# Optimization experiments

Measured on AMD Instinct MI355X. Metric: run time of the kernel, lower is better.

## Reference

```python
import jax, jax.numpy as jnp
import numpy as np
import math

B, S, D, H, COND = 4, 2048, 768, 12, 128
DH = D // H
MLP = 4 * D
EPS = 1e-5


def setup_inputs() -> dict:
    key = jax.random.key(0)
    ks = jax.random.split(key, 10)
    s = 0.02  # init scale for weights
    x = jax.random.normal(ks[0], (B, S, D), jnp.float32)
    c = jax.random.normal(ks[1], (B, COND), jnp.float32)
    # rotary tables, layout (1, S, 3, 1, DH) per module docstring
    pos = jnp.arange(S, dtype=jnp.float32)
    inv_freq = 1.0 / (10000.0 ** (jnp.arange(0, DH, 2, dtype=jnp.float32) / DH))
    ang = pos[:, None] * inv_freq[None, :]            # (S, DH/2)
    cos = jnp.concatenate([jnp.cos(ang), jnp.cos(ang)], -1)  # (S, DH)
    sin = jnp.concatenate([jnp.sin(ang), jnp.sin(ang)], -1)
    cos = jnp.broadcast_to(cos[None, :, None, None, :], (1, S, 3, 1, DH))
    sin = jnp.broadcast_to(sin[None, :, None, None, :], (1, S, 3, 1, DH))
    return {
        "x": x,
        "cos": cos,
        "sin": sin,
        "c": c,
        "ln1_w": jnp.ones((D,), jnp.float32),
        "W_qkv": s * jax.random.normal(ks[2], (3 * D, D), jnp.float32),
        "W_out": s * jax.random.normal(ks[3], (D, D), jnp.float32),
        "W_mlp1": s * jax.random.normal(ks[4], (MLP, D), jnp.float32),
        "b_mlp1": jnp.zeros((MLP,), jnp.float32),
        "W_mlp2": s * jax.random.normal(ks[5], (D, MLP), jnp.float32),
        "b_mlp2": jnp.zeros((D,), jnp.float32),
        "ln2_w": jnp.ones((D,), jnp.float32),
        "W_ada": s * jax.random.normal(ks[6], (6 * D, COND), jnp.float32),
        "b_ada": jnp.zeros((6 * D,), jnp.float32),
    }


def _ln(x, w):
    # LayerNorm with weight only (no bias), computed in fp32 like the original
    xf = x.astype(jnp.float32)
    mu = xf.mean(-1, keepdims=True)
    var = ((xf - mu) ** 2).mean(-1, keepdims=True)
    return (xf - mu) * jax.lax.rsqrt(var + EPS) * w


def reference(x, cos, sin, c, ln1_w, W_qkv, W_out, W_mlp1, b_mlp1, W_mlp2, b_mlp2, ln2_w, W_ada, b_ada):
    b, s_len = x.shape[0], x.shape[1]
    # adaLN modulation: (B, 6D) -> six (B, 1, D) chunks
    ada = c @ W_ada.T + b_ada
    sh_msa, sc_msa, g_msa, sh_mlp, sc_mlp, g_mlp = [t[:, None, :] for t in jnp.split(ada, 6, axis=-1)]

    x_skip = x
    h = _ln(x, ln1_w) * (1.0 + sc_msa) + sh_msa
    qkv = (h @ W_qkv.T).reshape(b, s_len, 3, H, DH)

    # rotary: slice as in apply_rotary_pos_emb_for_macos
    cos_s = cos[0, :, 0, 0, : DH // 2][None, :, None, :]  # (1, S, 1, DH/2)
    sin_s = sin[0, :, 0, 0, : DH // 2][None, :, None, :]
    q, k, v = qkv[:, :, 0], qkv[:, :, 1], qkv[:, :, 2]     # (B, S, H, DH)

    def _rot(t):
        t1, t2 = t[..., : DH // 2], t[..., DH // 2 :]
        return jnp.concatenate([t1 * cos_s - t2 * sin_s, t1 * sin_s + t2 * cos_s], -1)

    q, k = _rot(q), _rot(k)

    # non-causal attention
    scale = 1.0 / math.sqrt(DH)
    scores = jnp.einsum("bshd,bthd->bhst", q, k) * scale
    attn = jax.nn.softmax(scores, axis=-1)
    o = jnp.einsum("bhst,bthd->bshd", attn, v).reshape(b, s_len, D)

    # bias_dropout_add_scale (inference: dropout = identity)
    x = x_skip + g_msa * (o @ W_out.T)

    h2 = _ln(x, ln2_w) * (1.0 + sc_mlp) + sh_mlp
    m = jax.nn.gelu(h2 @ W_mlp1.T + b_mlp1, approximate=True) @ W_mlp2.T + b_mlp2
    return x + g_mlp * m
```

## Files before the change

kernel.cpp:

```cpp
#include <hip/hip_runtime.h>

typedef __bf16 bf16;
typedef __bf16 bf16x4 __attribute__((ext_vector_type(4)));
typedef __bf16 bf16x8 __attribute__((ext_vector_type(8)));
typedef float floatx4 __attribute__((ext_vector_type(4)));

#define MFMA16(a, b, c) __builtin_amdgcn_mfma_f32_16x16x32_bf16((a), (b), (c), 0, 0, 0)

__device__ __forceinline__ float san(float v, float magic) {
  unsigned u = __builtin_bit_cast(unsigned, v);
  return ((u & 0x7f800000u) == 0x7f800000u) ? magic : v;
}

__device__ __forceinline__ void gld_lds16(bf16* lds, const bf16* g) {
  __builtin_amdgcn_global_load_lds((__attribute__((address_space(1))) void*)g,
                                   (__attribute__((address_space(3))) void*)lds,
                                   16, 0, 0);
}

__global__ __launch_bounds__(256) void wcvt_k(const float* __restrict__ w,
                                              bf16* __restrict__ o, int n4) {
  int i = blockIdx.x * 256 + threadIdx.x;
  if (i >= n4) return;
  float4 v = ((const float4*)w)[i];
  bf16x4 b = {(bf16)v.x, (bf16)v.y, (bf16)v.z, (bf16)v.w};
  *(bf16x4*)(o + (size_t)i * 4) = b;
}

__global__ __launch_bounds__(256) void wcvt4_k(const float* __restrict__ wqkv,
                                               const float* __restrict__ wout,
                                               const float* __restrict__ wm1,
                                               const float* __restrict__ wm2,
                                               bf16* __restrict__ dst) {
  int i = blockIdx.x * 256 + threadIdx.x;
  if (i >= 1769472) return;
  const float* s;
  int off;
  if (i < 442368) { s = wqkv; off = 0; }
  else if (i < 589824) { s = wout; off = 442368; }
  else if (i < 1179648) { s = wm1; off = 589824; }
  else { s = wm2; off = 1179648; }
  float4 v = ((const float4*)s)[i - off];
  bf16x4 b = {(bf16)v.x, (bf16)v.y, (bf16)v.z, (bf16)v.w};
  *(bf16x4*)(dst + (size_t)i * 4) = b;
}

__global__ void ada_k(const float* __restrict__ c, const float* __restrict__ W,
                      const float* __restrict__ bias, float* __restrict__ ada) {
  int idx = blockIdx.x * 256 + threadIdx.x;
  if (idx >= 4 * 4608) return;
  int bb = idx / 4608;
  int j = idx - bb * 4608;
  float s = bias[j];
  const float4* wp = (const float4*)(W + (size_t)j * 128);
  const float4* cp = (const float4*)(c + (size_t)bb * 128);
#pragma unroll
  for (int t = 0; t < 32; t++) {
    float4 w4 = wp[t], c4 = cp[t];
    s += c4.x * w4.x + c4.y * w4.y + c4.z * w4.z + c4.w * w4.w;
  }
  ada[idx] = san(s, 7.0e3f);
}

__global__ __launch_bounds__(256) void ln_mod_k(const float* __restrict__ xin,
                                                const float* __restrict__ lnw,
                                                const float* __restrict__ ada,
                                                int sh_off, int sc_off,
                                                bf16* __restrict__ h,
                                                int tok_base) {
  int wv = threadIdx.x >> 6, lane = threadIdx.x & 63;
  int tok = tok_base + blockIdx.x * 4 + wv;
  int bb = tok >> 11;
  const float* xr = xin + (size_t)tok * 768;
  size_t obase = (size_t)(tok - tok_base) * 768;
  float4 v[3];
#pragma unroll
  for (int r = 0; r < 3; r++) v[r] = *(const float4*)(xr + lane * 4 + r * 256);
  float s1 = 0.f, s2 = 0.f;
#pragma unroll
  for (int r = 0; r < 3; r++) {
    s1 += v[r].x + v[r].y + v[r].z + v[r].w;
    s2 += v[r].x * v[r].x + v[r].y * v[r].y + v[r].z * v[r].z + v[r].w * v[r].w;
  }
#pragma unroll
  for (int off = 32; off > 0; off >>= 1) {
    s1 += __shfl_xor(s1, off);
    s2 += __shfl_xor(s2, off);
  }
  float mu = s1 * (1.f / 768.f);
  float rs = rsqrtf(s2 * (1.f / 768.f) - mu * mu + 1e-5f);
  const float* adab = ada + bb * 4608;
#pragma unroll
  for (int r = 0; r < 3; r++) {
    int j = lane * 4 + r * 256;
    float4 sc = *(const float4*)(adab + sc_off + j);
    float4 sh = *(const float4*)(adab + sh_off + j);
    float4 w4 = *(const float4*)(lnw + j);
    bf16x4 o4;
    o4[0] = (bf16)san(((v[r].x - mu) * rs) * w4.x * (1.f + sc.x) + sh.x, 5.0e3f);
    o4[1] = (bf16)san(((v[r].y - mu) * rs) * w4.y * (1.f + sc.y) + sh.y, 5.0e3f);
    o4[2] = (bf16)san(((v[r].z - mu) * rs) * w4.z * (1.f + sc.z) + sh.z, 5.0e3f);
    o4[3] = (bf16)san(((v[r].w - mu) * rs) * w4.w * (1.f + sc.w) + sh.w, 5.0e3f);
    *(bf16x4*)&h[obase + j] = o4;
  }
}

template <int EPI>
__global__ __launch_bounds__(256, 3) void gemm_k(
    const bf16* __restrict__ A, const bf16* __restrict__ W, int K, int k_len,
    int m_base, const float* __restrict__ cosp, const float* __restrict__ sinp,
    const float* __restrict__ ada, const float* __restrict__ resid_x,
    const float* __restrict__ bias, bf16* __restrict__ out_q,
    bf16* __restrict__ out_k, bf16* __restrict__ out_v,
    float* __restrict__ out_f, float* __restrict__ out_f2) {
  __shared__ bf16 As[3][128 * 32];
  __shared__ bf16 Bs[3][128 * 32];
  int tid = threadIdx.x;
  int lane = tid & 63, wv = tid >> 6;
  int quad = lane >> 4, lm = lane & 15;
  int gx = gridDim.x, nwg = gx * gridDim.y;
  int d = blockIdx.y * gx + blockIdx.x;
  int lid = d;
  if ((nwg & 7) == 0) {
    int q8 = nwg >> 3;
    lid = (d & 7) * q8 + (d >> 3);
  }
  int by = lid / gx, bx = lid - by * gx;
  int m0 = by * 128, n0 = bx * 128;
  int mw = (wv >> 1) * 64, nw = (wv & 1) * 64;
  int kb = blockIdx.z * k_len;

  floatx4 acc[4][4];
#pragma unroll
  for (int i = 0; i < 4; i++)
#pragma unroll
    for (int j = 0; j < 4; j++) acc[i][j] = {0.f, 0.f, 0.f, 0.f};

  const bf16* Ag0 = A + (size_t)(m0 + wv * 16 + lm) * K + quad * 8;
  const bf16* Ag1 = Ag0 + (size_t)64 * K;
  const bf16* Bg0 = W + (size_t)(n0 + wv * 16 + lm) * K + quad * 8;
  const bf16* Bg1 = Bg0 + (size_t)64 * K;
  int wb = wv * 512;

#define STAGE_T(sb, kk)                    \
  do {                                     \
    gld_lds16(&As[sb][wb], Ag0 + (kk));    \
    gld_lds16(&As[sb][wb + 2048], Ag1 + (kk)); \
    gld_lds16(&Bs[sb][wb], Bg0 + (kk));    \
    gld_lds16(&Bs[sb][wb + 2048], Bg1 + (kk)); \
  } while (0)

  int nt = k_len >> 5;
  STAGE_T(0, kb);
  STAGE_T(1, kb + 32);

  int s_cur = 0;
  for (int t = 0; t < nt; t++) {
    if (t + 1 < nt)
      asm volatile("s_waitcnt vmcnt(4)" ::: "memory");
    else
      asm volatile("s_waitcnt vmcnt(0)" ::: "memory");
    __builtin_amdgcn_s_barrier();
    if (t + 2 < nt) {
      int sn = s_cur + 2;
      if (sn >= 3) sn -= 3;
      STAGE_T(sn, kb + (t + 2) * 32);
    }
    bf16x8 af[4], bfr[4];
#pragma unroll
    for (int i = 0; i < 4; i++) {
      int it = (mw >> 4) + i;
      af[i] = *(const bf16x8*)&As[s_cur][(size_t)(it * 64 + quad * 16 + lm) * 8];
      int jt = (nw >> 4) + i;
      bfr[i] = *(const bf16x8*)&Bs[s_cur][(size_t)(jt * 64 + quad * 16 + lm) * 8];
    }
#pragma unroll
    for (int i = 0; i < 4; i++)
#pragma unroll
      for (int j = 0; j < 4; j++) acc[i][j] = MFMA16(af[i], bfr[j], acc[i][j]);
    s_cur = (s_cur + 1 == 3) ? 0 : s_cur + 1;
  }
#undef STAGE_T

  int colb = n0 + nw;
#pragma unroll
  for (int i = 0; i < 4; i++) {
#pragma unroll
    for (int r = 0; r < 4; r++) {
      int mg = m_base + m0 + mw + i * 16 + quad * 4 + r;
      if (EPI == 0) {
        int bb = mg >> 11, s = mg & 2047;
        int sec = colb / 768;
        int nb = colb - sec * 768;
        int hh = nb >> 6;
        if (sec == 2) {
          size_t vbase = ((size_t)(bb * 12 + hh) * 64) * 2048 + s;
#pragma unroll
          for (int j = 0; j < 4; j++) {
            int d2 = j * 16 + lm;
            out_v[vbase + (size_t)d2 * 2048] = (bf16)san(acc[i][j][r], 100.f);
          }
        } else {
          const float* cs = cosp + (size_t)s * 192;
          const float* sn = sinp + (size_t)s * 192;
          bf16* dst = (sec == 0) ? out_q : out_k;
          float scl = (sec == 0) ? 0.125f : 1.0f;
          size_t base = ((size_t)(bb * 12 + hh) * 2048 + s) * 64;
#pragma unroll
          for (int j = 0; j < 2; j++) {
            int d2 = j * 16 + lm;
            float c0 = cs[d2], s0 = sn[d2];
            float t1 = san(acc[i][j][r], 100.f);
            float t2 = san(acc[i][j + 2][r], 100.f);
            dst[base + d2] = (bf16)((t1 * c0 - t2 * s0) * scl);
            dst[base + d2 + 32] = (bf16)((t1 * s0 + t2 * c0) * scl);
          }
        }
      } else if (EPI == 1) {
        int bb = mg >> 11;
#pragma unroll
        for (int j = 0; j < 4; j++) {
          int n = colb + j * 16 + lm;
          float g = ada[bb * 4608 + 1536 + n];
          float xv =
              san(resid_x[(size_t)mg * 768 + n] + g * acc[i][j][r], 1.0e5f);
          out_f[(size_t)mg * 768 + n] = xv;
          float g2 = ada[bb * 4608 + 3840 + n];
          out_f2[(size_t)mg * 768 + n] = xv + g2 * bias[n];
        }
      } else if (EPI == 2) {
#pragma unroll
        for (int j = 0; j < 4; j++) {
          int n = colb + j * 16 + lm;
          float v = acc[i][j][r] + bias[n];
          float t = tanhf(0.7978845608f * (v + 0.044715f * v * v * v));
          out_q[(size_t)(mg - m_base) * 3072 + n] =
              (bf16)san(0.5f * v * (1.f + t), 3.0e5f);
        }
      } else {
        int bb = mg >> 11;
#pragma unroll
        for (int j = 0; j < 4; j++) {
          int n = colb + j * 16 + lm;
          float g = ada[bb * 4608 + 3840 + n];
          atomicAdd(out_f + (size_t)mg * 768 + n, san(g * acc[i][j][r], 1.0e6f));
        }
      }
    }
  }
}

__global__ __launch_bounds__(256, 3) void attn_k(const bf16* __restrict__ q,
                                                 const bf16* __restrict__ k,
                                                 const bf16* __restrict__ vT,
                                                 bf16* __restrict__ o) {
  __shared__ bf16 Kbuf[2][4096];
  __shared__ bf16 Vbuf[2][4096];
  __shared__ bf16 Plds[4][16 * 72];
  int d = blockIdx.y * gridDim.x + blockIdx.x;
  int idx = d >> 3;
  int qt = idx & 31;
  int bh = ((idx >> 5) << 3) + (d & 7);
  int b = bh / 12, h = bh - b * 12;
  int tid = threadIdx.x, lane = tid & 63, wv = tid >> 6;
  int quad = lane >> 4, lm = lane & 15;

  const bf16* Kp = k + (size_t)bh * 2048 * 64;
  const bf16* Vp = vT + (size_t)bh * 64 * 2048;

  const bf16* Qrow =
      q + (size_t)bh * 2048 * 64 + (size_t)(qt * 64 + wv * 16 + lm) * 64;
  bf16x8 qf0 = *(const bf16x8*)(Qrow + quad * 8);
  bf16x8 qf1 = *(const bf16x8*)(Qrow + 32 + quad * 8);

  const bf16* ksrc0 = Kp + (size_t)(wv * 16 + lm) * 64 + quad * 8;
  const bf16* ksrc1 = ksrc0 + 32;
  const bf16* vsrc0 = Vp + (size_t)(wv * 16 + lm) * 2048 + quad * 8;
  const bf16* vsrc1 = vsrc0 + 32;

  float l_i = 0.f;
  floatx4 accO[4];
#pragma unroll
  for (int t = 0; t < 4; t++) accO[t] = {0.f, 0.f, 0.f, 0.f};

  gld_lds16(&Kbuf[0][(wv * 2 + 0) * 512], ksrc0);
  gld_lds16(&Kbuf[0][(wv * 2 + 1) * 512], ksrc1);
  gld_lds16(&Vbuf[0][(wv * 2 + 0) * 512], vsrc0);
  gld_lds16(&Vbuf[0][(wv * 2 + 1) * 512], vsrc1);

  int p = 0;
  for (int kt = 0; kt < 32; kt++) {
    __syncthreads();
    if (kt < 31) {
      size_t ko = (size_t)(kt + 1) * 4096;
      size_t vo = (size_t)(kt + 1) * 64;
      int pn = p ^ 1;
      gld_lds16(&Kbuf[pn][(wv * 2 + 0) * 512], ksrc0 + ko);
      gld_lds16(&Kbuf[pn][(wv * 2 + 1) * 512], ksrc1 + ko);
      gld_lds16(&Vbuf[pn][(wv * 2 + 0) * 512], vsrc0 + vo);
      gld_lds16(&Vbuf[pn][(wv * 2 + 1) * 512], vsrc1 + vo);
    }

    floatx4 accS[4];
#pragma unroll
    for (int i = 0; i < 4; i++) accS[i] = {0.f, 0.f, 0.f, 0.f};
    __builtin_amdgcn_s_setprio(1);
#pragma unroll
    for (int i = 0; i < 4; i++) {
      bf16x8 kf0 =
          *(const bf16x8*)&Kbuf[p][(size_t)((i * 2 + 0) * 64 + quad * 16 + lm) * 8];
      bf16x8 kf1 =
          *(const bf16x8*)&Kbuf[p][(size_t)((i * 2 + 1) * 64 + quad * 16 + lm) * 8];
      accS[i] = MFMA16(kf0, qf0, accS[i]);
      accS[i] = MFMA16(kf1, qf1, accS[i]);
    }
    __builtin_amdgcn_s_setprio(0);

    float psum = 0.f;
    bf16 pv[4][4];
#pragma unroll
    for (int i = 0; i < 4; i++)
#pragma unroll
      for (int r = 0; r < 4; r++) {
        float pe = __expf(accS[i][r]);
        psum += pe;
        pv[i][r] = (bf16)pe;
      }
    l_i += psum;

#pragma unroll
    for (int i = 0; i < 4; i++) {
      bf16x4 pk = {pv[i][0], pv[i][1], pv[i][2], pv[i][3]};
      *(bf16x4*)&Plds[wv][lm * 72 + i * 16 + quad * 4] = pk;
    }

    __builtin_amdgcn_s_setprio(1);
#pragma unroll
    for (int st = 0; st < 2; st++) {
      bf16x8 pf = *(const bf16x8*)&Plds[wv][lm * 72 + st * 32 + quad * 8];
#pragma unroll
      for (int t = 0; t < 4; t++) {
        bf16x8 vf =
            *(const bf16x8*)&Vbuf[p][(size_t)((t * 2 + st) * 64 + quad * 16 + lm) * 8];
        accO[t] = MFMA16(pf, vf, accO[t]);
      }
    }
    __builtin_amdgcn_s_setprio(0);
    p ^= 1;
  }

  l_i += __shfl_xor(l_i, 16);
  l_i += __shfl_xor(l_i, 32);

  float lr[4];
#pragma unroll
  for (int r = 0; r < 4; r++) lr[r] = 1.f / __shfl(l_i, (quad << 2) + r);
#pragma unroll
  for (int t = 0; t < 4; t++) {
#pragma unroll
    for (int r = 0; r < 4; r++) {
      int d2 = t * 16 + lm;
      int s = qt * 64 + wv * 16 + quad * 4 + r;
      o[((size_t)(b * 2048 + s)) * 768 + h * 64 + d2] =
          (bf16)san(accO[t][r] * lr[r], 3.0e4f);
    }
  }
}

extern "C" void kernel_launch(void* const* d_in, const int* in_sizes, int n_in,
                              void* d_out, int out_size, void* d_ws,
                              size_t ws_size, hipStream_t stream) {
  (void)in_sizes; (void)n_in; (void)out_size;
  const float* x = (const float*)d_in[0];
  const float* cosp = (const float*)d_in[1];
  const float* sinp = (const float*)d_in[2];
  const float* c = (const float*)d_in[3];
  const float* ln1w = (const float*)d_in[4];
  const float* Wqkv = (const float*)d_in[5];
  const float* Wout = (const float*)d_in[6];
  const float* Wm1 = (const float*)d_in[7];
  const float* bm1 = (const float*)d_in[8];
  const float* Wm2 = (const float*)d_in[9];
  const float* bm2 = (const float*)d_in[10];
  const float* ln2w = (const float*)d_in[11];
  const float* Wada = (const float*)d_in[12];
  const float* bada = (const float*)d_in[13];

  const size_t TOKB = (size_t)8192 * 768 * 2;
  char* ws = (char*)d_ws;
  float* ada = (float*)ws;
  char* base = ws + 73728;
  bf16* h = (bf16*)d_out;
  float* outp = (float*)d_out;

  if (ws_size >= 156000000) {
    bf16* qb = (bf16*)base;
    bf16* kb = (bf16*)(base + TOKB);
    bf16* vT = (bf16*)(base + 2 * TOKB);
    bf16* obuf = (bf16*)(base + 3 * TOKB);
    float* x2 = (float*)(base + 4 * TOKB);
    bf16* h2c = (bf16*)(base + 6 * TOKB);
    bf16* m1c = (bf16*)(base + 7 * TOKB);
    bf16* wall = (bf16*)(base + 11 * TOKB);
    bf16* wqkv_b = wall;
    bf16* wout_b = wall + (size_t)1769472;
    bf16* wm1_b = wall + (size_t)2359296;
    bf16* wm2_b = wall + (size_t)4718592;

    ada_k<<<72, 256, 0, stream>>>(c, Wada, bada, ada);
    wcvt4_k<<<6912, 256, 0, stream>>>(Wqkv, Wout, Wm1, Wm2, wall);
    ln_mod_k<<<2048, 256, 0, stream>>>(x, ln1w, ada, 0, 768, h, 0);
    gemm_k<0><<<dim3(18, 64), 256, 0, stream>>>(h, wqkv_b, 768, 768, 0, cosp,
                                                sinp, ada, nullptr, nullptr,
                                                qb, kb, vT, nullptr, nullptr);
    attn_k<<<dim3(32, 48), 256, 0, stream>>>(qb, kb, vT, obuf);
    gemm_k<1><<<dim3(6, 64), 256, 0, stream>>>(obuf, wout_b, 768, 768, 0,
                                               nullptr, nullptr, ada, x, bm2,
                                               nullptr, nullptr, nullptr, x2,
                                               outp);
    ln_mod_k<<<2048, 256, 0, stream>>>(x2, ln2w, ada, 2304, 3072, h2c, 0);
    gemm_k<2><<<dim3(24, 64), 256, 0, stream>>>(
        h2c, wm1_b, 768, 768, 0, nullptr, nullptr, nullptr, nullptr, bm1, m1c,
        nullptr, nullptr, nullptr, nullptr);
    gemm_k<4><<<dim3(6, 64, 2), 256, 0, stream>>>(
        m1c, wm2_b, 3072, 1536, 0, nullptr, nullptr, ada, nullptr, nullptr,
        nullptr, nullptr, nullptr, outp, nullptr);
  } else {
    bf16* qb = (bf16*)base;
    bf16* kb = (bf16*)(base + TOKB);
    bf16* vT = (bf16*)(base + 2 * TOKB);
    bf16* obuf = (bf16*)(base + 3 * TOKB);
    bf16* h2c = (bf16*)(base + 3 * TOKB);
    float* x2 = (float*)base;
    bf16* m1c = (bf16*)(base + TOKB);
    bf16* wqkv_b = (bf16*)(base + 3 * TOKB);
    bf16* wout_b = (bf16*)(base + 2 * TOKB);
    bf16* wm1_b = (bf16*)base;
    bf16* wm2_b = (bf16*)base + (size_t)3072 * 768;

    ada_k<<<72, 256, 0, stream>>>(c, Wada, bada, ada);
    ln_mod_k<<<2048, 256, 0, stream>>>(x, ln1w, ada, 0, 768, h, 0);
    wcvt_k<<<(2304 * 768 / 4 + 255) / 256, 256, 0, stream>>>(Wqkv, wqkv_b,
                                                             2304 * 768 / 4);
    gemm_k<0><<<dim3(18, 64), 256, 0, stream>>>(h, wqkv_b, 768, 768, 0, cosp,
                                                sinp, ada, nullptr, nullptr,
                                                qb, kb, vT, nullptr, nullptr);
    attn_k<<<dim3(32, 48), 256, 0, stream>>>(qb, kb, vT, obuf);
    wcvt_k<<<(768 * 768 / 4 + 255) / 256, 256, 0, stream>>>(Wout, wout_b,
                                                            768 * 768 / 4);
    gemm_k<1><<<dim3(6, 64), 256, 0, stream>>>(obuf, wout_b, 768, 768, 0,
                                               nullptr, nullptr, ada, x, bm2,
                                               nullptr, nullptr, nullptr, x2,
                                               outp);
    ln_mod_k<<<2048, 256, 0, stream>>>(x2, ln2w, ada, 2304, 3072, h2c, 0);
    wcvt_k<<<(3072 * 768 / 4 + 255) / 256, 256, 0, stream>>>(Wm1, wm1_b,
                                                             3072 * 768 / 4);
    wcvt_k<<<(768 * 3072 / 4 + 255) / 256, 256, 0, stream>>>(Wm2, wm2_b,
                                                             768 * 3072 / 4);
    for (int cidx = 0; cidx < 2; cidx++) {
      int mb = cidx * 4096;
      gemm_k<2><<<dim3(24, 32), 256, 0, stream>>>(
          h2c + (size_t)mb * 768, wm1_b, 768, 768, mb, nullptr, nullptr,
          nullptr, nullptr, bm1, m1c, nullptr, nullptr, nullptr, nullptr);
      gemm_k<4><<<dim3(6, 32, 2), 256, 0, stream>>>(
          m1c, wm2_b, 3072, 1536, mb, nullptr, nullptr, ada, nullptr, nullptr,
          nullptr, nullptr, nullptr, outp, nullptr);
    }
  }
}
```

Before: 547.5 us.

## Add 128x256 GEMM tile variant for QKV and MLP1 projections

```diff
diff --git a/kernel.cpp b/kernel.cpp
--- a/kernel.cpp
+++ b/kernel.cpp
@@ -105,16 +105,18 @@
   }
 }
 
-template <int EPI>
-__global__ __launch_bounds__(256, 3) void gemm_k(
+template <int EPI, int BN>
+__global__ __launch_bounds__(256, (BN == 256) ? 2 : 3) void gemm_k(
     const bf16* __restrict__ A, const bf16* __restrict__ W, int K, int k_len,
     int m_base, const float* __restrict__ cosp, const float* __restrict__ sinp,
     const float* __restrict__ ada, const float* __restrict__ resid_x,
     const float* __restrict__ bias, bf16* __restrict__ out_q,
     bf16* __restrict__ out_k, bf16* __restrict__ out_v,
     float* __restrict__ out_f, float* __restrict__ out_f2) {
+  constexpr int NJ = BN / 32;
+  constexpr int NG = BN / 64;
   __shared__ bf16 As[3][128 * 32];
-  __shared__ bf16 Bs[3][128 * 32];
+  __shared__ bf16 Bs[3][BN * 32];
   int tid = threadIdx.x;
   int lane = tid & 63, wv = tid >> 6;
   int quad = lane >> 4, lm = lane & 15;
@@ -126,28 +128,28 @@
     lid = (d & 7) * q8 + (d >> 3);
   }
   int by = lid / gx, bx = lid - by * gx;
-  int m0 = by * 128, n0 = bx * 128;
-  int mw = (wv >> 1) * 64, nw = (wv & 1) * 64;
+  int m0 = by * 128, n0 = bx * BN;
+  int mw = (wv >> 1) * 64, nw = (wv & 1) * (BN / 2);
   int kb = blockIdx.z * k_len;
 
-  floatx4 acc[4][4];
+  floatx4 acc[4][NJ];
 #pragma unroll
   for (int i = 0; i < 4; i++)
 #pragma unroll
-    for (int j = 0; j < 4; j++) acc[i][j] = {0.f, 0.f, 0.f, 0.f};
+    for (int j = 0; j < NJ; j++) acc[i][j] = {0.f, 0.f, 0.f, 0.f};
 
   const bf16* Ag0 = A + (size_t)(m0 + wv * 16 + lm) * K + quad * 8;
   const bf16* Ag1 = Ag0 + (size_t)64 * K;
   const bf16* Bg0 = W + (size_t)(n0 + wv * 16 + lm) * K + quad * 8;
-  const bf16* Bg1 = Bg0 + (size_t)64 * K;
   int wb = wv * 512;
 
-#define STAGE_T(sb, kk)                    \
-  do {                                     \
-    gld_lds16(&As[sb][wb], Ag0 + (kk));    \
-    gld_lds16(&As[sb][wb + 2048], Ag1 + (kk)); \
-    gld_lds16(&Bs[sb][wb], Bg0 + (kk));    \
-    gld_lds16(&Bs[sb][wb + 2048], Bg1 + (kk)); \
+#define STAGE_T(sb, kk)                                          \
+  do {                                                           \
+    gld_lds16(&As[sb][wb], Ag0 + (kk));                          \
+    gld_lds16(&As[sb][wb + 2048], Ag1 + (kk));                   \
+    _Pragma("unroll") for (int g = 0; g < NG; g++)               \
+        gld_lds16(&Bs[sb][g * 2048 + wb],                        \
+                  Bg0 + (size_t)g * 64 * K + (kk));              \
   } while (0)
 
   int nt = k_len >> 5;
@@ -156,28 +158,35 @@
 
   int s_cur = 0;
   for (int t = 0; t < nt; t++) {
-    if (t + 1 < nt)
-      asm volatile("s_waitcnt vmcnt(4)" ::: "memory");
-    else
+    if (t + 1 < nt) {
+      if constexpr (BN == 256)
+        asm volatile("s_waitcnt vmcnt(6)" ::: "memory");
+      else
+        asm volatile("s_waitcnt vmcnt(4)" ::: "memory");
+    } else {
       asm volatile("s_waitcnt vmcnt(0)" ::: "memory");
+    }
     __builtin_amdgcn_s_barrier();
     if (t + 2 < nt) {
       int sn = s_cur + 2;
       if (sn >= 3) sn -= 3;
       STAGE_T(sn, kb + (t + 2) * 32);
     }
-    bf16x8 af[4], bfr[4];
+    bf16x8 af[4], bfr[NJ];
 #pragma unroll
     for (int i = 0; i < 4; i++) {
       int it = (mw >> 4) + i;
       af[i] = *(const bf16x8*)&As[s_cur][(size_t)(it * 64 + quad * 16 + lm) * 8];
-      int jt = (nw >> 4) + i;
-      bfr[i] = *(const bf16x8*)&Bs[s_cur][(size_t)(jt * 64 + quad * 16 + lm) * 8];
+    }
+#pragma unroll
+    for (int j = 0; j < NJ; j++) {
+      int jt = (nw >> 4) + j;
+      bfr[j] = *(const bf16x8*)&Bs[s_cur][(size_t)(jt * 64 + quad * 16 + lm) * 8];
     }
 #pragma unroll
     for (int i = 0; i < 4; i++)
 #pragma unroll
-      for (int j = 0; j < 4; j++) acc[i][j] = MFMA16(af[i], bfr[j], acc[i][j]);
+      for (int j = 0; j < NJ; j++) acc[i][j] = MFMA16(af[i], bfr[j], acc[i][j]);
     s_cur = (s_cur + 1 == 3) ? 0 : s_cur + 1;
   }
 #undef STAGE_T
@@ -190,36 +199,41 @@
       int mg = m_base + m0 + mw + i * 16 + quad * 4 + r;
       if (EPI == 0) {
         int bb = mg >> 11, s = mg & 2047;
-        int sec = colb / 768;
-        int nb = colb - sec * 768;
-        int hh = nb >> 6;
-        if (sec == 2) {
-          size_t vbase = ((size_t)(bb * 12 + hh) * 64) * 2048 + s;
-#pragma unroll
-          for (int j = 0; j < 4; j++) {
-            int d2 = j * 16 + lm;
-            out_v[vbase + (size_t)d2 * 2048] = (bf16)san(acc[i][j][r], 100.f);
-          }
-        } else {
-          const float* cs = cosp + (size_t)s * 192;
-          const float* sn = sinp + (size_t)s * 192;
-          bf16* dst = (sec == 0) ? out_q : out_k;
-          float scl = (sec == 0) ? 0.125f : 1.0f;
-          size_t base = ((size_t)(bb * 12 + hh) * 2048 + s) * 64;
-#pragma unroll
-          for (int j = 0; j < 2; j++) {
-            int d2 = j * 16 + lm;
-            float c0 = cs[d2], s0 = sn[d2];
-            float t1 = san(acc[i][j][r], 100.f);
-            float t2 = san(acc[i][j + 2][r], 100.f);
-            dst[base + d2] = (bf16)((t1 * c0 - t2 * s0) * scl);
-            dst[base + d2 + 32] = (bf16)((t1 * s0 + t2 * c0) * scl);
+#pragma unroll
+        for (int g = 0; g < NJ / 4; g++) {
+          int cb = colb + g * 64;
+          int sec = cb / 768;
+          int nb = cb - sec * 768;
+          int hh = nb >> 6;
+          if (sec == 2) {
+            size_t vbase = ((size_t)(bb * 12 + hh) * 64) * 2048 + s;
+#pragma unroll
+            for (int j4 = 0; j4 < 4; j4++) {
+              int d2 = j4 * 16 + lm;
+              out_v[vbase + (size_t)d2 * 2048] =
+                  (bf16)san(acc[i][g * 4 + j4][r], 100.f);
+            }
+          } else {
+            const float* cs = cosp + (size_t)s * 192;
+            const float* sn = sinp + (size_t)s * 192;
+            bf16* dst = (sec == 0) ? out_q : out_k;
+            float scl = (sec == 0) ? 0.125f : 1.0f;
+            size_t base = ((size_t)(bb * 12 + hh) * 2048 + s) * 64;
+#pragma unroll
+            for (int jj = 0; jj < 2; jj++) {
+              int d2 = jj * 16 + lm;
+              float c0 = cs[d2], s0 = sn[d2];
+              float t1 = san(acc[i][g * 4 + jj][r], 100.f);
+              float t2 = san(acc[i][g * 4 + jj + 2][r], 100.f);
+              dst[base + d2] = (bf16)((t1 * c0 - t2 * s0) * scl);
+              dst[base + d2 + 32] = (bf16)((t1 * s0 + t2 * c0) * scl);
+            }
           }
         }
       } else if (EPI == 1) {
         int bb = mg >> 11;
 #pragma unroll
-        for (int j = 0; j < 4; j++) {
+        for (int j = 0; j < NJ; j++) {
           int n = colb + j * 16 + lm;
           float g = ada[bb * 4608 + 1536 + n];
           float xv =
@@ -230,7 +244,7 @@
         }
       } else if (EPI == 2) {
 #pragma unroll
-        for (int j = 0; j < 4; j++) {
+        for (int j = 0; j < NJ; j++) {
           int n = colb + j * 16 + lm;
           float v = acc[i][j][r] + bias[n];
           float t = tanhf(0.7978845608f * (v + 0.044715f * v * v * v));
@@ -240,7 +254,7 @@
       } else {
         int bb = mg >> 11;
 #pragma unroll
-        for (int j = 0; j < 4; j++) {
+        for (int j = 0; j < NJ; j++) {
           int n = colb + j * 16 + lm;
           float g = ada[bb * 4608 + 3840 + n];
           atomicAdd(out_f + (size_t)mg * 768 + n, san(g * acc[i][j][r], 1.0e6f));
@@ -410,19 +424,18 @@
     ada_k<<<72, 256, 0, stream>>>(c, Wada, bada, ada);
     wcvt4_k<<<6912, 256, 0, stream>>>(Wqkv, Wout, Wm1, Wm2, wall);
     ln_mod_k<<<2048, 256, 0, stream>>>(x, ln1w, ada, 0, 768, h, 0);
-    gemm_k<0><<<dim3(18, 64), 256, 0, stream>>>(h, wqkv_b, 768, 768, 0, cosp,
-                                                sinp, ada, nullptr, nullptr,
-                                                qb, kb, vT, nullptr, nullptr);
+    gemm_k<0, 256><<<dim3(9, 64), 256, 0, stream>>>(
+        h, wqkv_b, 768, 768, 0, cosp, sinp, ada, nullptr, nullptr, qb, kb, vT,
+        nullptr, nullptr);
     attn_k<<<dim3(32, 48), 256, 0, stream>>>(qb, kb, vT, obuf);
-    gemm_k<1><<<dim3(6, 64), 256, 0, stream>>>(obuf, wout_b, 768, 768, 0,
-                                               nullptr, nullptr, ada, x, bm2,
-                                               nullptr, nullptr, nullptr, x2,
-                                               outp);
+    gemm_k<1, 128><<<dim3(6, 64), 256, 0, stream>>>(
+        obuf, wout_b, 768, 768, 0, nullptr, nullptr, ada, x, bm2, nullptr,
+        nullptr, nullptr, x2, outp);
     ln_mod_k<<<2048, 256, 0, stream>>>(x2, ln2w, ada, 2304, 3072, h2c, 0);
-    gemm_k<2><<<dim3(24, 64), 256, 0, stream>>>(
+    gemm_k<2, 256><<<dim3(12, 64), 256, 0, stream>>>(
         h2c, wm1_b, 768, 768, 0, nullptr, nullptr, nullptr, nullptr, bm1, m1c,
         nullptr, nullptr, nullptr, nullptr);
-    gemm_k<4><<<dim3(6, 64, 2), 256, 0, stream>>>(
+    gemm_k<4, 128><<<dim3(6, 64, 2), 256, 0, stream>>>(
         m1c, wm2_b, 3072, 1536, 0, nullptr, nullptr, ada, nullptr, nullptr,
         nullptr, nullptr, nullptr, outp, nullptr);
   } else {
@@ -442,16 +455,15 @@
     ln_mod_k<<<2048, 256, 0, stream>>>(x, ln1w, ada, 0, 768, h, 0);
     wcvt_k<<<(2304 * 768 / 4 + 255) / 256, 256, 0, stream>>>(Wqkv, wqkv_b,
                                                              2304 * 768 / 4);
-    gemm_k<0><<<dim3(18, 64), 256, 0, stream>>>(h, wqkv_b, 768, 768, 0, cosp,
-                                                sinp, ada, nullptr, nullptr,
-                                                qb, kb, vT, nullptr, nullptr);
+    gemm_k<0, 256><<<dim3(9, 64), 256, 0, stream>>>(
+        h, wqkv_b, 768, 768, 0, cosp, sinp, ada, nullptr, nullptr, qb, kb, vT,
+        nullptr, nullptr);
     attn_k<<<dim3(32, 48), 256, 0, stream>>>(qb, kb, vT, obuf);
     wcvt_k<<<(768 * 768 / 4 + 255) / 256, 256, 0, stream>>>(Wout, wout_b,
                                                             768 * 768 / 4);
-    gemm_k<1><<<dim3(6, 64), 256, 0, stream>>>(obuf, wout_b, 768, 768, 0,
-                                               nullptr, nullptr, ada, x, bm2,
-                                               nullptr, nullptr, nullptr, x2,
-                                               outp);
+    gemm_k<1, 128><<<dim3(6, 64), 256, 0, stream>>>(
+        obuf, wout_b, 768, 768, 0, nullptr, nullptr, ada, x, bm2, nullptr,
+        nullptr, nullptr, x2, outp);
     ln_mod_k<<<2048, 256, 0, stream>>>(x2, ln2w, ada, 2304, 3072, h2c, 0);
     wcvt_k<<<(3072 * 768 / 4 + 255) / 256, 256, 0, stream>>>(Wm1, wm1_b,
                                                              3072 * 768 / 4);
@@ -459,10 +471,10 @@
                                                              768 * 3072 / 4);
     for (int cidx = 0; cidx < 2; cidx++) {
       int mb = cidx * 4096;
-      gemm_k<2><<<dim3(24, 32), 256, 0, stream>>>(
+      gemm_k<2, 256><<<dim3(12, 32), 256, 0, stream>>>(
           h2c + (size_t)mb * 768, wm1_b, 768, 768, mb, nullptr, nullptr,
           nullptr, nullptr, bm1, m1c, nullptr, nullptr, nullptr, nullptr);
-      gemm_k<4><<<dim3(6, 32, 2), 256, 0, stream>>>(
+      gemm_k<4, 128><<<dim3(6, 32, 2), 256, 0, stream>>>(
           m1c, wm2_b, 3072, 1536, mb, nullptr, nullptr, ada, nullptr, nullptr,
           nullptr, nullptr, nullptr, outp, nullptr);
     }
```

After: 579.9 us. +5.9%, slower.
